# Kernel optimization log

Hardware: AMD Instinct MI355X
Metric: run time of the kernel (lower is better)

## Reference

```python
import jax, jax.numpy as jnp
import numpy as np

EPS = 1e-12  # F.normalize default eps


def setup_inputs() -> dict:
    key = jax.random.key(0)
    k1, k2, k3, k4 = jax.random.split(key, 4)
    B, C, H, W = 8, 256, 128, 128
    N, T = 100, 6
    return {
        "visual_features": jax.random.normal(k1, (B, C, H, W), dtype=jnp.float32),
        "text_embeddings": jax.random.normal(k2, (T, C), dtype=jnp.float32),
        "masks": jax.random.uniform(k3, (B, N, H, W), dtype=jnp.float32),
        "class_labels": jax.random.randint(k4, (B, N), 0, 7),
        "temperature": jnp.asarray(0.07, dtype=jnp.float32),
    }


def reference(visual_features, text_embeddings, masks, class_labels, temperature):
    # visual_features: (B,C,H,W); text_embeddings: (T,C); masks: (B,N,H,W); class_labels: (B,N)
    T = text_embeddings.shape[0]
    # masks already at (H,W): bilinear resize to same size is identity -> just threshold
    mask_bin = (masks > 0.5).astype(visual_features.dtype)          # (B,N,H,W), detached
    mask_bin = jax.lax.stop_gradient(mask_bin)
    msum = mask_bin.sum(axis=(2, 3))                                 # (B,N)
    # masked sum-pool then mean (clamp denom at 1, as in torch)
    pooled = jnp.einsum('bchw,bnhw->bnc', visual_features, mask_bin)
    pooled = pooled / jnp.maximum(msum, 1.0)[..., None]              # (B,N,C)
    pooled = pooled / jnp.maximum(jnp.linalg.norm(pooled, axis=-1, keepdims=True), EPS)
    text_norm = text_embeddings / jnp.maximum(
        jnp.linalg.norm(text_embeddings, axis=-1, keepdims=True), EPS)
    sims = jnp.einsum('bnc,tc->bnt', pooled, text_norm) / jnp.abs(temperature)  # (B,N,T)
    logp = jax.nn.log_softmax(sims, axis=-1)
    tgt = jnp.clip(class_labels - 1, 0, T - 1)
    ce = -jnp.take_along_axis(logp, tgt[..., None], axis=-1)[..., 0]  # (B,N)
    valid = ((class_labels >= 1) & (class_labels <= T) & (msum >= 1.0)).astype(ce.dtype)
    cnt = valid.sum()
    loss = jnp.where(cnt > 0, (ce * valid).sum() / jnp.maximum(cnt, 1.0),
                     jnp.asarray(0.0, ce.dtype))
    return loss
```

## Files before the change

kernel.cpp:

```cpp
#include <hip/hip_runtime.h>
#include <hip/hip_bf16.h>
#include <stdint.h>

constexpr int cB  = 8;
constexpr int cC  = 256;
constexpr int cHW = 128 * 128;
constexpr int cN  = 100;
constexpr int cT  = 6;
constexpr int NPAD = 112;
constexpr int WPB = cHW / 32;
constexpr int KSLICES = 32;
constexpr int PXS = cHW / KSLICES;
constexpr int NWIN = PXS / 32;
constexpr int NGRP = NWIN / 4;
constexpr int NBLK = cB * 16 * (KSLICES / 4);

typedef __attribute__((ext_vector_type(8))) short short8;
typedef __attribute__((ext_vector_type(4))) float floatx4;

__device__ __forceinline__ unsigned pack2(float a, float b) {
    const __hip_bfloat16 ha = __float2bfloat16(a);
    const __hip_bfloat16 hb = __float2bfloat16(b);
    return (unsigned)__builtin_bit_cast(unsigned short, ha)
         | ((unsigned)__builtin_bit_cast(unsigned short, hb) << 16);
}

__global__ __launch_bounds__(256)
void mask_prep_kernel(const float* __restrict__ masks,
                      unsigned* __restrict__ bits, unsigned* __restrict__ msum)
{
    const int t = threadIdx.x, lane = t & 63, w = t >> 6;
    const int b = blockIdx.x / NPAD;
    const int n = blockIdx.x % NPAD;
    unsigned* dst = bits + ((size_t)b * NPAD + n) * WPB;

    if (n >= cN) {
        *(uint2*)(dst + t * 2) = make_uint2(0u, 0u);
        return;
    }
    const float* src = masks + ((size_t)b * cN + n) * cHW + w * 4096;
    unsigned* wdst = dst + w * 128;
    int pc = 0;
    #pragma unroll
    for (int r = 0; r < 16; ++r) {
        const floatx4 v = *(const floatx4*)(src + r * 256 + lane * 4);
        const bool b0 = v.x > 0.5f, b1 = v.y > 0.5f, b2 = v.z > 0.5f, b3 = v.w > 0.5f;
        const unsigned long long B0 = __ballot(b0), B1 = __ballot(b1),
                                 B2 = __ballot(b2), B3 = __ballot(b3);
        pc += (int)b0 + (int)b1 + (int)b2 + (int)b3;
        if (lane < 8) {
            const int sh = lane * 8;
            const unsigned word =
                  (unsigned)((B0 >> sh) & 0xFFull)
                | ((unsigned)((B1 >> sh) & 0xFFull) << 8)
                | ((unsigned)((B2 >> sh) & 0xFFull) << 16)
                | ((unsigned)((B3 >> sh) & 0xFFull) << 24);
            wdst[r * 8 + lane] = word;
        }
    }
    #pragma unroll
    for (int off = 32; off > 0; off >>= 1) pc += __shfl_xor(pc, off, 64);
    __shared__ int ps[4];
    if (lane == 0) ps[w] = pc;
    __syncthreads();
    if (t == 0) msum[b * cN + n] = (unsigned)(ps[0] + ps[1] + ps[2] + ps[3]);
}

template<bool USE_PART>
__global__ __launch_bounds__(256)
void pool_kernel(const float* __restrict__ vf, const unsigned* __restrict__ bits,
                 float* __restrict__ part, float* __restrict__ pooled)
{
    __shared__ float red[4][28][64];

    const int tid  = threadIdx.x;
    const int lane = tid & 63;
    const int widx = tid >> 6;
    const int bid  = blockIdx.x;
    const int b    = bid >> 7;
    const int ct   = (bid >> 3) & 15;
    const int kg   = bid & 7;
    const int ks   = kg * 4 + widx;
    const int l15  = lane & 15;
    const int lk   = lane >> 4;
    const int lk2  = lk * 2;
    const int p0   = ks * PXS;

    const float* vrow = vf + ((size_t)(b * cC + ct * 16 + l15)) * cHW + p0 + lk * 8;
    const unsigned* brow = bits + ((size_t)b * NPAD + l15) * WPB + (p0 >> 5);

    floatx4 acc[7];
    #pragma unroll
    for (int mt = 0; mt < 7; ++mt) acc[mt] = (floatx4){0.f, 0.f, 0.f, 0.f};

    floatx4 vr[4][2];
    #pragma unroll
    for (int u = 0; u < 4; ++u) {
        vr[u][0] = *(const floatx4*)(vrow + u * 32);
        vr[u][1] = *(const floatx4*)(vrow + u * 32 + 4);
    }
    uint4 bwA[7], bwB[7];
    #pragma unroll
    for (int mt = 0; mt < 7; ++mt)
        bwA[mt] = *(const uint4*)(brow + (size_t)mt * 16 * WPB);

    auto GROUP = [&](int g, uint4 (&bw)[7], uint4 (&bwn)[7]) {
        if (g < NGRP - 1) {
            #pragma unroll
            for (int mt = 0; mt < 7; ++mt)
                bwn[mt] = *(const uint4*)(brow + (size_t)mt * 16 * WPB + (g + 1) * 4);
        }
        #pragma unroll
        for (int u = 0; u < 4; ++u) {
            const int w = g * 4 + u;
            union { short8 s8; uint4 u4; } bq;
            bq.u4.x = pack2(vr[u][0].x, vr[u][0].y);
            bq.u4.y = pack2(vr[u][0].z, vr[u][0].w);
            bq.u4.z = pack2(vr[u][1].x, vr[u][1].y);
            bq.u4.w = pack2(vr[u][1].z, vr[u][1].w);
            if (g < NGRP - 1) {
                vr[u][0] = *(const floatx4*)(vrow + (w + 4) * 32);
                vr[u][1] = *(const floatx4*)(vrow + (w + 4) * 32 + 4);
            }
            #pragma unroll
            for (int mt = 0; mt < 7; ++mt) {
                const unsigned word = (u == 0) ? bw[mt].x : (u == 1) ? bw[mt].y
                                    : (u == 2) ? bw[mt].z : bw[mt].w;
                const unsigned te = (word >> lk2) & 0x01010101u;
                const unsigned to = (word >> (lk2 + 1)) & 0x01010101u;
                union { short8 s8; uint4 u4; } aq;
                aq.u4.x = __umul24(__builtin_amdgcn_perm(0u, te, 0x04010400u), 0x3F80u);
                aq.u4.y = __umul24(__builtin_amdgcn_perm(0u, te, 0x04030402u), 0x3F80u);
                aq.u4.z = __umul24(__builtin_amdgcn_perm(0u, to, 0x04010400u), 0x3F80u);
                aq.u4.w = __umul24(__builtin_amdgcn_perm(0u, to, 0x04030402u), 0x3F80u);
                acc[mt] = __builtin_amdgcn_mfma_f32_16x16x32_bf16(aq.s8, bq.s8, acc[mt], 0, 0, 0);
            }
        }
    };

    GROUP(0, bwA, bwB);
    GROUP(1, bwB, bwA);
    GROUP(2, bwA, bwB);
    GROUP(3, bwB, bwA);

    #pragma unroll
    for (int mt = 0; mt < 7; ++mt)
        #pragma unroll
        for (int i = 0; i < 4; ++i)
            red[widx][mt * 4 + i][lane] = acc[mt][i];
    __syncthreads();

    float s[7];
    #pragma unroll
    for (int mt = 0; mt < 7; ++mt) {
        const int e = mt * 4 + widx;
        s[mt] = red[0][e][lane] + red[1][e][lane] + red[2][e][lane] + red[3][e][lane];
    }

    if (USE_PART) {
        float* dst = part + (size_t)bid * (cN * 16);
        #pragma unroll
        for (int mt = 0; mt < 7; ++mt) {
            const int n = mt * 16 + (lane >> 4) * 4 + widx;
            if (n < cN) dst[n * 16 + l15] = s[mt];
        }
    } else {
        #pragma unroll
        for (int mt = 0; mt < 7; ++mt) {
            const int n = mt * 16 + (lane >> 4) * 4 + widx;
            if (n < cN)
                atomicAdd(&pooled[((size_t)b * cN + n) * cC + ct * 16 + l15], s[mt]);
        }
    }
}

__device__ __forceinline__ float wred(float v) {
    #pragma unroll
    for (int off = 32; off > 0; off >>= 1) v += __shfl_xor(v, off, 64);
    return v;
}

template<bool USE_PART>
__global__ __launch_bounds__(256)
void finalize_kernel(const float* __restrict__ pp, const unsigned* __restrict__ msum,
                     const float* __restrict__ text, const int* __restrict__ labels,
                     const float* __restrict__ temp, float* __restrict__ bpart)
{
    const int lane = threadIdx.x & 63;
    const int wv   = threadIdx.x >> 6;
    const int row  = blockIdx.x * 4 + wv;
    const int b = row / cN, n = row % cN;

    floatx4 p = (floatx4){0.f, 0.f, 0.f, 0.f};
    if (USE_PART) {
        const int ct  = lane >> 2;
        const int col = (lane & 3) * 4;
        const float* src = pp + ((size_t)(b * 16 + ct) * 8) * (cN * 16) + n * 16 + col;
        #pragma unroll
        for (int kg = 0; kg < 8; ++kg)
            p += *(const floatx4*)(src + (size_t)kg * (cN * 16));
    } else {
        p = *(const floatx4*)(pp + (size_t)row * cC + lane * 4);
    }

    const float m   = (float)msum[row];
    const float inv = 1.0f / fmaxf(m, 1.0f);
    p.x *= inv; p.y *= inv; p.z *= inv; p.w *= inv;

    const int c_global = USE_PART ? ((lane >> 2) * 16 + (lane & 3) * 4) : lane * 4;

    float psq = p.x * p.x + p.y * p.y + p.z * p.z + p.w * p.w;
    float dot[cT], tsq[cT];
    #pragma unroll
    for (int t = 0; t < cT; ++t) {
        const floatx4 x = *(const floatx4*)(text + (size_t)t * cC + c_global);
        dot[t] = p.x * x.x + p.y * x.y + p.z * x.z + p.w * x.w;
        tsq[t] = x.x * x.x + x.y * x.y + x.z * x.z + x.w * x.w;
    }
    psq = wred(psq);
    #pragma unroll
    for (int t = 0; t < cT; ++t) { dot[t] = wred(dot[t]); tsq[t] = wred(tsq[t]); }

    __shared__ float lce[4], lcnt[4];
    if (lane == 0) {
        const float tempv = fabsf(temp[0]);
        const float pn = fmaxf(sqrtf(psq), 1e-12f);
        float sims[cT], mx = -1e30f;
        #pragma unroll
        for (int t = 0; t < cT; ++t) {
            sims[t] = dot[t] / (pn * fmaxf(sqrtf(tsq[t]), 1e-12f)) / tempv;
            mx = fmaxf(mx, sims[t]);
        }
        float se = 0.f;
        #pragma unroll
        for (int t = 0; t < cT; ++t) se += expf(sims[t] - mx);
        const float lse = logf(se);

        const int lab = labels[row];
        const int tgt = min(max(lab - 1, 0), cT - 1);
        const float ce = -(sims[tgt] - mx - lse);
        const bool valid = (lab >= 1) && (lab <= cT) && (m >= 1.0f);
        lce[wv]  = valid ? ce : 0.f;
        lcnt[wv] = valid ? 1.f : 0.f;
    }
    __syncthreads();
    if (threadIdx.x == 0) {
        bpart[blockIdx.x * 2]     = lce[0] + lce[1] + lce[2] + lce[3];
        bpart[blockIdx.x * 2 + 1] = lcnt[0] + lcnt[1] + lcnt[2] + lcnt[3];
    }
}

__global__ __launch_bounds__(256)
void loss_kernel(const float* __restrict__ bp, float* __restrict__ out) {
    const int t = threadIdx.x, lane = t & 63, w = t >> 6;
    float ce = 0.f, cnt = 0.f;
    if (t < 200) { ce = bp[t * 2]; cnt = bp[t * 2 + 1]; }
    ce = wred(ce); cnt = wred(cnt);
    __shared__ float a[8];
    if (lane == 0) { a[w * 2] = ce; a[w * 2 + 1] = cnt; }
    __syncthreads();
    if (t == 0) {
        const float s = a[0] + a[2] + a[4] + a[6];
        const float c = a[1] + a[3] + a[5] + a[7];
        out[0] = (c > 0.f) ? s / fmaxf(c, 1.f) : 0.f;
    }
}

__global__ void zero_kernel(float* __restrict__ p, int n) {
    const int i = blockIdx.x * 256 + threadIdx.x;
    if (i < n) p[i] = 0.f;
}

extern "C" void kernel_launch(void* const* d_in, const int* in_sizes, int n_in,
                              void* d_out, int out_size, void* d_ws, size_t ws_size,
                              hipStream_t stream)
{
    const float* vf     = (const float*)d_in[0];
    const float* text   = (const float*)d_in[1];
    const float* masks  = (const float*)d_in[2];
    const int*   labels = (const int*)d_in[3];
    const float* temp   = (const float*)d_in[4];

    float*    wsf   = (float*)d_ws;
    float*    bpart = wsf;
    unsigned* msum  = (unsigned*)(wsf + 512);

    const size_t PART_FLOATS = (size_t)NBLK * cN * 16;
    const size_t BITS_WORDS  = (size_t)cB * NPAD * WPB;

    const bool use_part =
        ws_size >= (4096 + PART_FLOATS + BITS_WORDS + 64) * sizeof(float);

    if (use_part) {
        float*    part = wsf + 4096;
        unsigned* bits = (unsigned*)(wsf + 4096 + PART_FLOATS);
        hipLaunchKernelGGL(mask_prep_kernel, dim3(cB * NPAD), dim3(256), 0, stream,
                           masks, bits, msum);
        hipLaunchKernelGGL((pool_kernel<true>), dim3(NBLK), dim3(256), 0, stream,
                           vf, bits, part, nullptr);
        hipLaunchKernelGGL((finalize_kernel<true>), dim3(cB * cN / 4), dim3(256), 0, stream,
                           part, msum, text, labels, temp, bpart);
    } else {
        float*    pooled = wsf + 4096;
        unsigned* bits   = (unsigned*)(wsf + 4096 + (size_t)cB * cN * cC);
        hipLaunchKernelGGL(zero_kernel, dim3((cB * cN * cC + 255) / 256), dim3(256), 0, stream,
                           pooled, cB * cN * cC);
        hipLaunchKernelGGL(mask_prep_kernel, dim3(cB * NPAD), dim3(256), 0, stream,
                           masks, bits, msum);
        hipLaunchKernelGGL((pool_kernel<false>), dim3(NBLK), dim3(256), 0, stream,
                           vf, bits, nullptr, pooled);
        hipLaunchKernelGGL((finalize_kernel<false>), dim3(cB * cN / 4), dim3(256), 0, stream,
                           pooled, msum, text, labels, temp, bpart);
    }
    hipLaunchKernelGGL(loss_kernel, dim3(1), dim3(256), 0, stream,
                       bpart, (float*)d_out);
}
```

Before: 55.24 us.

## Double K-slices, fuse loss reduction into finalize, precompute text norms

The number of pixel slices per image doubles, giving twice as many pool blocks with half the work each, and the occupancy hint rises to 8 blocks per CU. The cross-wave reduction now uses a two-step tree with a smaller shared buffer. The separate loss kernel is removed: the last finalize block, found through an atomic counter, does the final reduction. Text normalization moves into an extra block of the mask prep kernel. Together these cut one launch and add parallelism in the main kernel, at the cost of twice the partial-sum traffic and the removal of the atomic fallback path when workspace is small.

```diff
diff --git a/kernel.cpp b/kernel.cpp
--- a/kernel.cpp
+++ b/kernel.cpp
@@ -9,7 +9,7 @@
 constexpr int cT  = 6;
 constexpr int NPAD = 112;
 constexpr int WPB = cHW / 32;
-constexpr int KSLICES = 32;
+constexpr int KSLICES = 64;
 constexpr int PXS = cHW / KSLICES;
 constexpr int NWIN = PXS / 32;
 constexpr int NGRP = NWIN / 4;
@@ -25,19 +25,45 @@
          | ((unsigned)__builtin_bit_cast(unsigned short, hb) << 16);
 }
 
+__device__ __forceinline__ float wred(float v) {
+    #pragma unroll
+    for (int off = 32; off > 0; off >>= 1) v += __shfl_xor(v, off, 64);
+    return v;
+}
+
 __global__ __launch_bounds__(256)
-void mask_prep_kernel(const float* __restrict__ masks,
-                      unsigned* __restrict__ bits, unsigned* __restrict__ msum)
+void mask_prep_kernel(const float* __restrict__ masks, const float* __restrict__ text,
+                      unsigned* __restrict__ bits, unsigned* __restrict__ msum,
+                      float* __restrict__ tnorm, unsigned* __restrict__ fincnt)
 {
     const int t = threadIdx.x, lane = t & 63, w = t >> 6;
+
+    if (blockIdx.x == cB * NPAD) {
+        float v[cT], sq[cT];
+        #pragma unroll
+        for (int q = 0; q < cT; ++q) {
+            v[q] = text[q * cC + t];
+            sq[q] = wred(v[q] * v[q]);
+        }
+        __shared__ float ps[cT][4];
+        if (lane == 0)
+            #pragma unroll
+            for (int q = 0; q < cT; ++q) ps[q][w] = sq[q];
+        __syncthreads();
+        #pragma unroll
+        for (int q = 0; q < cT; ++q) {
+            const float nrm = fmaxf(sqrtf(ps[q][0] + ps[q][1] + ps[q][2] + ps[q][3]), 1e-12f);
+            tnorm[q * cC + t] = v[q] / nrm;
+        }
+        if (t == 0) *fincnt = 0u;
+        return;
+    }
+
     const int b = blockIdx.x / NPAD;
     const int n = blockIdx.x % NPAD;
     unsigned* dst = bits + ((size_t)b * NPAD + n) * WPB;
-
-    if (n >= cN) {
-        *(uint2*)(dst + t * 2) = make_uint2(0u, 0u);
-        return;
-    }
+    if (n >= cN) { *(uint2*)(dst + t * 2) = make_uint2(0u, 0u); return; }
+
     const float* src = masks + ((size_t)b * cN + n) * cHW + w * 4096;
     unsigned* wdst = dst + w * 128;
     int pc = 0;
@@ -60,31 +86,30 @@
     }
     #pragma unroll
     for (int off = 32; off > 0; off >>= 1) pc += __shfl_xor(pc, off, 64);
-    __shared__ int ps[4];
-    if (lane == 0) ps[w] = pc;
-    __syncthreads();
-    if (t == 0) msum[b * cN + n] = (unsigned)(ps[0] + ps[1] + ps[2] + ps[3]);
-}
-
-template<bool USE_PART>
-__global__ __launch_bounds__(256)
+    __shared__ int ps2[4];
+    if (lane == 0) ps2[w] = pc;
+    __syncthreads();
+    if (t == 0) msum[b * cN + n] = (unsigned)(ps2[0] + ps2[1] + ps2[2] + ps2[3]);
+}
+
+__global__ __launch_bounds__(256, 8)
 void pool_kernel(const float* __restrict__ vf, const unsigned* __restrict__ bits,
-                 float* __restrict__ part, float* __restrict__ pooled)
+                 float* __restrict__ part)
 {
-    __shared__ float red[4][28][64];
+    __shared__ float red[2][28][64];
 
     const int tid  = threadIdx.x;
     const int lane = tid & 63;
     const int widx = tid >> 6;
     const int bid  = blockIdx.x;
-    const int b    = bid >> 7;
-    const int ct   = (bid >> 3) & 15;
-    const int kg   = bid & 7;
-    const int ks   = kg * 4 + widx;
+    const int b    = bid >> 8;
+    const int ct   = (bid >> 4) & 15;
+    const int kg   = bid & 15;
+    const int sl   = kg * 4 + widx;
     const int l15  = lane & 15;
     const int lk   = lane >> 4;
     const int lk2  = lk * 2;
-    const int p0   = ks * PXS;
+    const int p0   = sl * PXS;
 
     const float* vrow = vf + ((size_t)(b * cC + ct * 16 + l15)) * cHW + p0 + lk * 8;
     const unsigned* brow = bits + ((size_t)b * NPAD + l15) * WPB + (p0 >> 5);
@@ -99,17 +124,13 @@
         vr[u][0] = *(const floatx4*)(vrow + u * 32);
         vr[u][1] = *(const floatx4*)(vrow + u * 32 + 4);
     }
-    uint4 bwA[7], bwB[7];
-    #pragma unroll
-    for (int mt = 0; mt < 7; ++mt)
-        bwA[mt] = *(const uint4*)(brow + (size_t)mt * 16 * WPB);
-
-    auto GROUP = [&](int g, uint4 (&bw)[7], uint4 (&bwn)[7]) {
-        if (g < NGRP - 1) {
-            #pragma unroll
-            for (int mt = 0; mt < 7; ++mt)
-                bwn[mt] = *(const uint4*)(brow + (size_t)mt * 16 * WPB + (g + 1) * 4);
-        }
+
+    #pragma unroll
+    for (int g = 0; g < NGRP; ++g) {
+        uint4 bw[7];
+        #pragma unroll
+        for (int mt = 0; mt < 7; ++mt)
+            bw[mt] = *(const uint4*)(brow + (size_t)mt * 16 * WPB + g * 4);
         #pragma unroll
         for (int u = 0; u < 4; ++u) {
             const int w = g * 4 + u;
@@ -136,90 +157,81 @@
                 acc[mt] = __builtin_amdgcn_mfma_f32_16x16x32_bf16(aq.s8, bq.s8, acc[mt], 0, 0, 0);
             }
         }
-    };
-
-    GROUP(0, bwA, bwB);
-    GROUP(1, bwB, bwA);
-    GROUP(2, bwA, bwB);
-    GROUP(3, bwB, bwA);
-
-    #pragma unroll
-    for (int mt = 0; mt < 7; ++mt)
-        #pragma unroll
-        for (int i = 0; i < 4; ++i)
-            red[widx][mt * 4 + i][lane] = acc[mt][i];
-    __syncthreads();
-
-    float s[7];
-    #pragma unroll
-    for (int mt = 0; mt < 7; ++mt) {
-        const int e = mt * 4 + widx;
-        s[mt] = red[0][e][lane] + red[1][e][lane] + red[2][e][lane] + red[3][e][lane];
-    }
-
-    if (USE_PART) {
+    }
+
+    if (widx & 1) {
+        #pragma unroll
+        for (int mt = 0; mt < 7; ++mt)
+            #pragma unroll
+            for (int i = 0; i < 4; ++i)
+                red[widx >> 1][mt * 4 + i][lane] = acc[mt][i];
+    }
+    __syncthreads();
+    if (!(widx & 1)) {
+        #pragma unroll
+        for (int mt = 0; mt < 7; ++mt)
+            #pragma unroll
+            for (int i = 0; i < 4; ++i)
+                acc[mt][i] += red[widx >> 1][mt * 4 + i][lane];
+    }
+    __syncthreads();
+    if (widx == 2) {
+        #pragma unroll
+        for (int mt = 0; mt < 7; ++mt)
+            #pragma unroll
+            for (int i = 0; i < 4; ++i)
+                red[0][mt * 4 + i][lane] = acc[mt][i];
+    }
+    __syncthreads();
+    if (widx == 0) {
         float* dst = part + (size_t)bid * (cN * 16);
         #pragma unroll
         for (int mt = 0; mt < 7; ++mt) {
-            const int n = mt * 16 + (lane >> 4) * 4 + widx;
-            if (n < cN) dst[n * 16 + l15] = s[mt];
-        }
-    } else {
-        #pragma unroll
-        for (int mt = 0; mt < 7; ++mt) {
-            const int n = mt * 16 + (lane >> 4) * 4 + widx;
-            if (n < cN)
-                atomicAdd(&pooled[((size_t)b * cN + n) * cC + ct * 16 + l15], s[mt]);
-        }
-    }
-}
-
-__device__ __forceinline__ float wred(float v) {
-    #pragma unroll
-    for (int off = 32; off > 0; off >>= 1) v += __shfl_xor(v, off, 64);
-    return v;
-}
-
-template<bool USE_PART>
+            #pragma unroll
+            for (int i = 0; i < 4; ++i) {
+                const float s = acc[mt][i] + red[0][mt * 4 + i][lane];
+                const int n = mt * 16 + lk * 4 + i;
+                if (n < cN) dst[n * 16 + l15] = s;
+            }
+        }
+    }
+}
+
 __global__ __launch_bounds__(256)
-void finalize_kernel(const float* __restrict__ pp, const unsigned* __restrict__ msum,
-                     const float* __restrict__ text, const int* __restrict__ labels,
-                     const float* __restrict__ temp, float* __restrict__ bpart)
+void finalize_kernel(const float* __restrict__ part, const unsigned* __restrict__ msum,
+                     const float* __restrict__ tnorm, const int* __restrict__ labels,
+                     const float* __restrict__ temp, float* __restrict__ bpart,
+                     unsigned* __restrict__ fincnt, float* __restrict__ out)
 {
-    const int lane = threadIdx.x & 63;
-    const int wv   = threadIdx.x >> 6;
+    const int tid  = threadIdx.x;
+    const int lane = tid & 63;
+    const int wv   = tid >> 6;
     const int row  = blockIdx.x * 4 + wv;
     const int b = row / cN, n = row % cN;
+    const int ct  = lane >> 2;
+    const int col = (lane & 3) * 4;
+    const int c_global = ct * 16 + col;
 
     floatx4 p = (floatx4){0.f, 0.f, 0.f, 0.f};
-    if (USE_PART) {
-        const int ct  = lane >> 2;
-        const int col = (lane & 3) * 4;
-        const float* src = pp + ((size_t)(b * 16 + ct) * 8) * (cN * 16) + n * 16 + col;
-        #pragma unroll
-        for (int kg = 0; kg < 8; ++kg)
-            p += *(const floatx4*)(src + (size_t)kg * (cN * 16));
-    } else {
-        p = *(const floatx4*)(pp + (size_t)row * cC + lane * 4);
-    }
+    const float* src = part + ((size_t)(b * 256 + ct * 16)) * (cN * 16) + n * 16 + col;
+    #pragma unroll
+    for (int kg = 0; kg < 16; ++kg)
+        p += *(const floatx4*)(src + (size_t)kg * (cN * 16));
 
     const float m   = (float)msum[row];
     const float inv = 1.0f / fmaxf(m, 1.0f);
     p.x *= inv; p.y *= inv; p.z *= inv; p.w *= inv;
 
-    const int c_global = USE_PART ? ((lane >> 2) * 16 + (lane & 3) * 4) : lane * 4;
-
     float psq = p.x * p.x + p.y * p.y + p.z * p.z + p.w * p.w;
-    float dot[cT], tsq[cT];
-    #pragma unroll
-    for (int t = 0; t < cT; ++t) {
-        const floatx4 x = *(const floatx4*)(text + (size_t)t * cC + c_global);
-        dot[t] = p.x * x.x + p.y * x.y + p.z * x.z + p.w * x.w;
-        tsq[t] = x.x * x.x + x.y * x.y + x.z * x.z + x.w * x.w;
+    float dot[cT];
+    #pragma unroll
+    for (int q = 0; q < cT; ++q) {
+        const floatx4 x = *(const floatx4*)(tnorm + (size_t)q * cC + c_global);
+        dot[q] = p.x * x.x + p.y * x.y + p.z * x.z + p.w * x.w;
     }
     psq = wred(psq);
     #pragma unroll
-    for (int t = 0; t < cT; ++t) { dot[t] = wred(dot[t]); tsq[t] = wred(tsq[t]); }
+    for (int q = 0; q < cT; ++q) dot[q] = wred(dot[q]);
 
     __shared__ float lce[4], lcnt[4];
     if (lane == 0) {
@@ -227,13 +239,13 @@
         const float pn = fmaxf(sqrtf(psq), 1e-12f);
         float sims[cT], mx = -1e30f;
         #pragma unroll
-        for (int t = 0; t < cT; ++t) {
-            sims[t] = dot[t] / (pn * fmaxf(sqrtf(tsq[t]), 1e-12f)) / tempv;
-            mx = fmaxf(mx, sims[t]);
+        for (int q = 0; q < cT; ++q) {
+            sims[q] = dot[q] / pn / tempv;
+            mx = fmaxf(mx, sims[q]);
         }
         float se = 0.f;
         #pragma unroll
-        for (int t = 0; t < cT; ++t) se += expf(sims[t] - mx);
+        for (int q = 0; q < cT; ++q) se += expf(sims[q] - mx);
         const float lse = logf(se);
 
         const int lab = labels[row];
@@ -244,31 +256,34 @@
         lcnt[wv] = valid ? 1.f : 0.f;
     }
     __syncthreads();
-    if (threadIdx.x == 0) {
+    if (tid == 0) {
         bpart[blockIdx.x * 2]     = lce[0] + lce[1] + lce[2] + lce[3];
         bpart[blockIdx.x * 2 + 1] = lcnt[0] + lcnt[1] + lcnt[2] + lcnt[3];
     }
-}
-
-__global__ __launch_bounds__(256)
-void loss_kernel(const float* __restrict__ bp, float* __restrict__ out) {
-    const int t = threadIdx.x, lane = t & 63, w = t >> 6;
-    float ce = 0.f, cnt = 0.f;
-    if (t < 200) { ce = bp[t * 2]; cnt = bp[t * 2 + 1]; }
-    ce = wred(ce); cnt = wred(cnt);
-    __shared__ float a[8];
-    if (lane == 0) { a[w * 2] = ce; a[w * 2 + 1] = cnt; }
-    __syncthreads();
-    if (t == 0) {
-        const float s = a[0] + a[2] + a[4] + a[6];
-        const float c = a[1] + a[3] + a[5] + a[7];
-        out[0] = (c > 0.f) ? s / fmaxf(c, 1.f) : 0.f;
-    }
-}
-
-__global__ void zero_kernel(float* __restrict__ p, int n) {
-    const int i = blockIdx.x * 256 + threadIdx.x;
-    if (i < n) p[i] = 0.f;
+
+    __threadfence();
+    __shared__ bool isLast;
+    if (tid == 0)
+        isLast = (__hip_atomic_fetch_add(fincnt, 1u, __ATOMIC_ACQ_REL,
+                                         __HIP_MEMORY_SCOPE_AGENT) == 199u);
+    __syncthreads();
+    if (isLast) {
+        __threadfence();
+        float ce = 0.f, cnt = 0.f;
+        if (tid < 200) {
+            ce  = __hip_atomic_load(&bpart[tid * 2],     __ATOMIC_RELAXED, __HIP_MEMORY_SCOPE_AGENT);
+            cnt = __hip_atomic_load(&bpart[tid * 2 + 1], __ATOMIC_RELAXED, __HIP_MEMORY_SCOPE_AGENT);
+        }
+        ce = wred(ce); cnt = wred(cnt);
+        __shared__ float a[8];
+        if (lane == 0) { a[wv * 2] = ce; a[wv * 2 + 1] = cnt; }
+        __syncthreads();
+        if (tid == 0) {
+            const float s = a[0] + a[2] + a[4] + a[6];
+            const float c = a[1] + a[3] + a[5] + a[7];
+            out[0] = (c > 0.f) ? s / fmaxf(c, 1.f) : 0.f;
+        }
+    }
 }
 
 extern "C" void kernel_launch(void* const* d_in, const int* in_sizes, int n_in,
@@ -281,37 +296,23 @@
     const int*   labels = (const int*)d_in[3];
     const float* temp   = (const float*)d_in[4];
 
-    float*    wsf   = (float*)d_ws;
-    float*    bpart = wsf;
-    unsigned* msum  = (unsigned*)(wsf + 512);
-
+    float*    wsf    = (float*)d_ws;
+    float*    bpart  = wsf;
+    unsigned* fincnt = (unsigned*)(wsf + 408);
+    float*    tnorm  = wsf + 512;
+    unsigned* msum   = (unsigned*)(wsf + 2048);
+    float*    part   = wsf + 4096;
     const size_t PART_FLOATS = (size_t)NBLK * cN * 16;
     const size_t BITS_WORDS  = (size_t)cB * NPAD * WPB;
-
-    const bool use_part =
-        ws_size >= (4096 + PART_FLOATS + BITS_WORDS + 64) * sizeof(float);
-
-    if (use_part) {
-        float*    part = wsf + 4096;
-        unsigned* bits = (unsigned*)(wsf + 4096 + PART_FLOATS);
-        hipLaunchKernelGGL(mask_prep_kernel, dim3(cB * NPAD), dim3(256), 0, stream,
-                           masks, bits, msum);
-        hipLaunchKernelGGL((pool_kernel<true>), dim3(NBLK), dim3(256), 0, stream,
-                           vf, bits, part, nullptr);
-        hipLaunchKernelGGL((finalize_kernel<true>), dim3(cB * cN / 4), dim3(256), 0, stream,
-                           part, msum, text, labels, temp, bpart);
-    } else {
-        float*    pooled = wsf + 4096;
-        unsigned* bits   = (unsigned*)(wsf + 4096 + (size_t)cB * cN * cC);
-        hipLaunchKernelGGL(zero_kernel, dim3((cB * cN * cC + 255) / 256), dim3(256), 0, stream,
-                           pooled, cB * cN * cC);
-        hipLaunchKernelGGL(mask_prep_kernel, dim3(cB * NPAD), dim3(256), 0, stream,
-                           masks, bits, msum);
-        hipLaunchKernelGGL((pool_kernel<false>), dim3(NBLK), dim3(256), 0, stream,
-                           vf, bits, nullptr, pooled);
-        hipLaunchKernelGGL((finalize_kernel<false>), dim3(cB * cN / 4), dim3(256), 0, stream,
-                           pooled, msum, text, labels, temp, bpart);
-    }
-    hipLaunchKernelGGL(loss_kernel, dim3(1), dim3(256), 0, stream,
-                       bpart, (float*)d_out);
-}
+    unsigned* bits   = (unsigned*)(wsf + 4096 + PART_FLOATS);
+
+    if (ws_size < (4096 + PART_FLOATS + BITS_WORDS + 64) * sizeof(float))
+        return;
+
+    hipLaunchKernelGGL(mask_prep_kernel, dim3(cB * NPAD + 1), dim3(256), 0, stream,
+                       masks, text, bits, msum, tnorm, fincnt);
+    hipLaunchKernelGGL(pool_kernel, dim3(NBLK), dim3(256), 0, stream,
+                       vf, bits, part);
+    hipLaunchKernelGGL(finalize_kernel, dim3(cB * cN / 4), dim3(256), 0, stream,
+                       part, msum, tnorm, labels, temp, bpart, fincnt, (float*)d_out);
+}
```

New measurement: 121.4 us. 2.2x slower.
